# Performance work log

Measured on AMD Instinct MI355X. Metric: run time of the kernel, lower is better.

The kernel has to match this reference:

```python
import jax, jax.numpy as jnp
import numpy as np

B, T, C = 4, 2048, 1024
H, HS = 16, 64  # num_heads, head_size; H*HS == C

def setup_inputs() -> dict:
    key = jax.random.key(0)
    ks = jax.random.split(key, 6)
    s = 0.02
    x = jax.random.normal(ks[0], (B, T, C), dtype=jnp.float32)
    Wq = jax.random.normal(ks[1], (H, C, HS), dtype=jnp.float32) * s
    Wk = jax.random.normal(ks[2], (H, C, HS), dtype=jnp.float32) * s
    Wv = jax.random.normal(ks[3], (H, C, HS), dtype=jnp.float32) * s
    Wproj = jax.random.normal(ks[4], (C, C), dtype=jnp.float32) * s  # applied as out @ Wproj
    bproj = jax.random.normal(ks[5], (C,), dtype=jnp.float32) * s
    return {"x": x, "Wq": Wq, "Wk": Wk, "Wv": Wv, "Wproj": Wproj, "bproj": bproj}

def reference(x, Wq, Wk, Wv, Wproj, bproj):
    Bx, Tx, Cx = x.shape
    scale = Cx ** (-0.5)  # NOTE: original scales by n_embd, not head_size
    q = jnp.einsum('btc,hcd->bhtd', x, Wq)
    k = jnp.einsum('btc,hcd->bhtd', x, Wk)
    v = jnp.einsum('btc,hcd->bhtd', x, Wv)
    wei = jnp.einsum('bhtd,bhsd->bhts', q, k) * scale  # [B,H,T,T]
    causal = jnp.tril(jnp.ones((Tx, Tx), dtype=bool))
    wei = jnp.where(causal, wei, -jnp.inf)
    wei = jax.nn.softmax(wei, axis=-1)
    out = jnp.einsum('bhts,bhsd->bhtd', wei, v)
    out = out.transpose(0, 2, 1, 3).reshape(Bx, Tx, Cx)  # concat heads
    return out @ Wproj + bproj
```

## Files before the change

kernel.cpp:

```cpp
#include <hip/hip_runtime.h>


using u16    = unsigned short;
using bf16x8 = __attribute__((ext_vector_type(8))) short;
using bf16x4 = __attribute__((ext_vector_type(4))) short;
using f32x4  = __attribute__((ext_vector_type(4))) float;

#define MFMA_BF16(a, b, c) __builtin_amdgcn_mfma_f32_16x16x32_bf16((a), (b), (c), 0, 0, 0)

__device__ __forceinline__ f32x4 mfma16(bf16x4 a, bf16x4 b, f32x4 c) {
#if __has_builtin(__builtin_amdgcn_mfma_f32_16x16x16bf16_1k)
    return __builtin_amdgcn_mfma_f32_16x16x16bf16_1k(a, b, c, 0, 0, 0);
#elif __has_builtin(__builtin_amdgcn_mfma_f32_16x16x16_bf16)
    return __builtin_amdgcn_mfma_f32_16x16x16_bf16(a, b, c, 0, 0, 0);
#else
    asm("v_mfma_f32_16x16x16_bf16 %0, %1, %2, %0" : "+v"(c) : "v"(a), "v"(b));
    return c;
#endif
}

__device__ __forceinline__ u16 f2bf(float f) {
    union { float f; unsigned u; } v; v.f = f;
    unsigned u = v.u;
    u += 0x7FFFu + ((u >> 16) & 1u);
    return (u16)(u >> 16);
}
__device__ __forceinline__ short tbf(float f) {
    union { float f; unsigned u; } v; v.f = f;
    return (short)(v.u >> 16);
}

__device__ __forceinline__ void gl_lds16(const void* g, void* s) {
    __builtin_amdgcn_global_load_lds(
        (__attribute__((address_space(1))) void*)g,
        (__attribute__((address_space(3))) void*)s,
        16, 0, 0);
}

__global__ void cvt_x(const float* __restrict__ x, u16* __restrict__ xb, int n4) {
    int i = blockIdx.x * blockDim.x + threadIdx.x;
    if (i < n4) {
        float4 v = ((const float4*)x)[i];
        ushort4 o;
        o.x = f2bf(v.x); o.y = f2bf(v.y); o.z = f2bf(v.z); o.w = f2bf(v.w);
        ((ushort4*)xb)[i] = o;
    }
}

__global__ void transpose_w(const float* __restrict__ Wq, const float* __restrict__ Wk,
                            const float* __restrict__ Wv, u16* __restrict__ WT) {
    __shared__ float tile[64][65];
    const int tid = threadIdx.x;
    const int c0  = blockIdx.x * 64;
    const int h   = blockIdx.y;
    const int z   = blockIdx.z;
    const float* W = (z == 0 ? Wq : (z == 1 ? Wk : Wv)) + (size_t)h * 1024 * 64;
    u16* out = WT + (size_t)z * 1024 * 1024 + (size_t)h * 64 * 1024;
    #pragma unroll
    for (int i = 0; i < 16; ++i) {
        int idx = i * 256 + tid;
        int r = idx >> 6, d = idx & 63;
        tile[d][r] = W[(size_t)(c0 + r) * 64 + d];
    }
    __syncthreads();
    #pragma unroll
    for (int i = 0; i < 16; ++i) {
        int idx = i * 256 + tid;
        int d = idx >> 6, j = idx & 63;
        out[(size_t)d * 1024 + c0 + j] = f2bf(tile[d][j]);
    }
}

__global__ void transpose_p(const float* __restrict__ Wp, u16* __restrict__ WpT) {
    __shared__ float tile[64][65];
    const int tid = threadIdx.x;
    const int c0  = blockIdx.x * 64;
    const int n0  = blockIdx.y * 64;
    #pragma unroll
    for (int i = 0; i < 16; ++i) {
        int idx = i * 256 + tid;
        int r = idx >> 6, j = idx & 63;
        tile[j][r] = Wp[(size_t)(c0 + r) * 1024 + n0 + j];
    }
    __syncthreads();
    #pragma unroll
    for (int i = 0; i < 16; ++i) {
        int idx = i * 256 + tid;
        int r = idx >> 6, j = idx & 63;
        WpT[(size_t)(n0 + r) * 1024 + c0 + j] = f2bf(tile[r][j]);
    }
}

template <int MODE>
__global__ __launch_bounds__(256, 2)
void gemm_bt(const u16* __restrict__ A, const u16* __restrict__ Bt,
             u16* __restrict__ Oq, u16* __restrict__ Ok, u16* __restrict__ Ov,
             float* __restrict__ Op, const float* __restrict__ bias) {
    constexpr int K = 1024;
    __shared__ u16 As[128 * 32];
    __shared__ u16 Bs[128 * 32];
    const int tid  = threadIdx.x;
    const int w    = tid >> 6;
    const int lane = tid & 63;
    const int quad = lane >> 4;
    const int l16  = lane & 15;
    const int m0   = blockIdx.x * 128;
    const int n0   = blockIdx.y * 128;
    const u16* Bp  = (MODE == 0) ? (Bt + (size_t)blockIdx.z * 1024 * 1024) : Bt;

    const f32x4 zero = {0.f, 0.f, 0.f, 0.f};
    f32x4 acc[4][4];
    #pragma unroll
    for (int i = 0; i < 4; ++i)
        #pragma unroll
        for (int j = 0; j < 4; ++j) acc[i][j] = zero;

    const int wr = (w >> 1) * 64;
    const int wc = (w & 1) * 64;

    for (int k0 = 0; k0 < K; k0 += 32) {
        __syncthreads();
        #pragma unroll
        for (int i = 0; i < 2; ++i) {
            int c = i * 256 + tid;
            int row = c >> 2, ko = (c & 3) * 8;
            gl_lds16(A + (size_t)(m0 + row) * K + (k0 + ko), &As[(i * 256 + w * 64) * 8]);
        }
        #pragma unroll
        for (int i = 0; i < 2; ++i) {
            int c = i * 256 + tid;
            int row = c >> 2, ko = (c & 3) * 8;
            gl_lds16(Bp + (size_t)(n0 + row) * K + (k0 + ko), &Bs[(i * 256 + w * 64) * 8]);
        }
        __syncthreads();
        bf16x8 af[4], bfr[4];
        #pragma unroll
        for (int i = 0; i < 4; ++i)
            af[i] = *(const bf16x8*)&As[(wr + i * 16 + l16) * 32 + quad * 8];
        #pragma unroll
        for (int j = 0; j < 4; ++j)
            bfr[j] = *(const bf16x8*)&Bs[(wc + j * 16 + l16) * 32 + quad * 8];
        #pragma unroll
        for (int i = 0; i < 4; ++i)
            #pragma unroll
            for (int j = 0; j < 4; ++j)
                acc[i][j] = MFMA_BF16(af[i], bfr[j], acc[i][j]);
    }

    #pragma unroll
    for (int i = 0; i < 4; ++i) {
        #pragma unroll
        for (int j = 0; j < 4; ++j) {
            #pragma unroll
            for (int r = 0; r < 4; ++r) {
                const int m = m0 + wr + i * 16 + quad * 4 + r;
                const int n = n0 + wc + j * 16 + l16;
                const float v = acc[i][j][r];
                if (MODE == 0) {
                    const int b = m >> 11, t = m & 2047;
                    const int h = n >> 6, d = n & 63;
                    const int bh = b * 16 + h;
                    if (blockIdx.z == 0)
                        Oq[((size_t)bh * 2048 + t) * 64 + d] = f2bf(v * 0.03125f);
                    else if (blockIdx.z == 1)
                        Ok[((size_t)bh * 2048 + t) * 64 + d] = f2bf(v);
                    else
                        Ov[((size_t)bh * 64 + d) * 2048 + t] = f2bf(v);
                } else {
                    Op[(size_t)m * 1024 + n] = v + bias[n];
                }
            }
        }
    }
}

__global__ __launch_bounds__(256, 2)
void attn7(const u16* __restrict__ Q, const u16* __restrict__ Kg,
           const u16* __restrict__ Vt, u16* __restrict__ O) {
    __shared__ __align__(16) u16 Ks[2][2 * 128 * 32];
    __shared__ __align__(16) u16 VF[16 * 128 * 4];
    const int tid  = threadIdx.x;
    const int w    = tid >> 6;
    const int lane = tid & 63;
    const int quad = lane >> 4;
    const int l16  = lane & 15;
    const int bh   = blockIdx.y;
    const u16* Qp = Q  + (size_t)bh * 2048 * 64;
    const u16* Kp = Kg + (size_t)bh * 2048 * 64;
    const u16* Vp = Vt + (size_t)bh * 64 * 2048;
    const int b = bh >> 4, h = bh & 15;
    const float NEG_INF = -__builtin_inff();
    const f32x4 zero = {0.f, 0.f, 0.f, 0.f};
    const int vd = w * 16 + l16;

    #pragma unroll
    for (int ph = 0; ph < 2; ++ph) {
        const int tt = ph ? (int)blockIdx.x : 15 - (int)blockIdx.x;
        const int t0 = tt * 128;
        const int ns = tt + 1;

        bf16x8 bq[2][2];
        #pragma unroll
        for (int tf = 0; tf < 2; ++tf)
            #pragma unroll
            for (int kk = 0; kk < 2; ++kk)
                bq[tf][kk] = *(const bf16x8*)(Qp + (size_t)(t0 + w * 32 + tf * 16 + l16) * 64
                                              + kk * 32 + quad * 8);

        f32x4 oacc[4][2];
        float lsum[2] = {0.f, 0.f};
        #pragma unroll
        for (int df = 0; df < 4; ++df)
            #pragma unroll
            for (int tf = 0; tf < 2; ++tf) oacc[df][tf] = zero;

        __syncthreads();
        uint4 vr[4];
        #pragma unroll
        for (int i = 0; i < 4; ++i) {
            int c = i * 256 + tid;
            int kk = c >> 9, row = (c >> 2) & 127, q4 = c & 3;
            gl_lds16(Kp + (size_t)row * 64 + kk * 32 + q4 * 8,
                     &Ks[0][(size_t)(i * 256 + w * 64) * 8]);
        }
        #pragma unroll
        for (int r = 0; r < 4; ++r)
            vr[r] = *(const uint4*)(Vp + (size_t)vd * 2048 + (r * 4 + quad) * 8);

        for (int it = 0; it < ns; ++it) {
            const int s0 = it * 128;
            const u16* Kc = Ks[it & 1];
            __syncthreads();
            #pragma unroll
            for (int r = 0; r < 4; ++r) {
                const int uA = ((w * 4 + r) * 128) + (quad & 1) * 64 + l16 * 2
                               + ((quad >> 1) & 1);
                *(uint2*)&VF[(size_t)uA * 4]        = make_uint2(vr[r].x, vr[r].y);
                *(uint2*)&VF[(size_t)(uA + 32) * 4] = make_uint2(vr[r].z, vr[r].w);
            }
            __syncthreads();

            if (it + 1 < ns) {
                const int sn = s0 + 128;
                u16* Kn = Ks[(it + 1) & 1];
                #pragma unroll
                for (int i = 0; i < 4; ++i) {
                    int c = i * 256 + tid;
                    int kk = c >> 9, row = (c >> 2) & 127, q4 = c & 3;
                    gl_lds16(Kp + (size_t)(sn + row) * 64 + kk * 32 + q4 * 8,
                             &Kn[(size_t)(i * 256 + w * 64) * 8]);
                }
                #pragma unroll
                for (int r = 0; r < 4; ++r)
                    vr[r] = *(const uint4*)(Vp + (size_t)vd * 2048 + sn + (r * 4 + quad) * 8);
            }

            const bool diag = (it == ns - 1);
            bf16x4 bp[8][2];
            #pragma unroll
            for (int st = 0; st < 8; ++st) {
                bf16x8 ak0 = *(const bf16x8*)&Kc[(st * 16 + l16) * 32 + quad * 8];
                bf16x8 ak1 = *(const bf16x8*)&Kc[(128 * 32) + (st * 16 + l16) * 32 + quad * 8];
                #pragma unroll
                for (int tf = 0; tf < 2; ++tf) {
                    f32x4 s = MFMA_BF16(ak0, bq[tf][0], zero);
                    s = MFMA_BF16(ak1, bq[tf][1], s);
                    if (diag) {
                        #pragma unroll
                        for (int r = 0; r < 4; ++r) {
                            int ss = s0 + st * 16 + quad * 4 + r;
                            int t  = t0 + w * 32 + tf * 16 + l16;
                            if (ss > t) s[r] = NEG_INF;
                        }
                    }
                    float p0 = __expf(s[0]), p1 = __expf(s[1]);
                    float p2 = __expf(s[2]), p3 = __expf(s[3]);
                    lsum[tf] += (p0 + p1) + (p2 + p3);
                    bf16x4 bb; bb[0] = tbf(p0); bb[1] = tbf(p1);
                    bb[2] = tbf(p2); bb[3] = tbf(p3);
                    bp[st][tf] = bb;
                }
            }
            #pragma unroll
            for (int kcp = 0; kcp < 4; ++kcp)
                #pragma unroll
                for (int df = 0; df < 4; ++df) {
                    bf16x8 av = *(const bf16x8*)&VF[(size_t)(((df * 4 + kcp) * 128)
                                                    + quad * 32 + l16 * 2) * 4];
                    bf16x4 alo = __builtin_shufflevector(av, av, 0, 1, 2, 3);
                    bf16x4 ahi = __builtin_shufflevector(av, av, 4, 5, 6, 7);
                    #pragma unroll
                    for (int tf = 0; tf < 2; ++tf) {
                        oacc[df][tf] = mfma16(alo, bp[2 * kcp][tf], oacc[df][tf]);
                        oacc[df][tf] = mfma16(ahi, bp[2 * kcp + 1][tf], oacc[df][tf]);
                    }
                }
        }

        #pragma unroll
        for (int tf = 0; tf < 2; ++tf) {
            float s = lsum[tf];
            s += __shfl_xor(s, 16, 64);
            s += __shfl_xor(s, 32, 64);
            lsum[tf] = 1.0f / s;
        }
        #pragma unroll
        for (int df = 0; df < 4; ++df)
            #pragma unroll
            for (int tf = 0; tf < 2; ++tf)
                #pragma unroll
                for (int r = 0; r < 4; ++r) {
                    int t = t0 + w * 32 + tf * 16 + l16;
                    int d = df * 16 + quad * 4 + r;
                    O[((size_t)(b * 2048 + t)) * 1024 + h * 64 + d]
                        = f2bf(oacc[df][tf][r] * lsum[tf]);
                }
    }
}

extern "C" void kernel_launch(void* const* d_in, const int* in_sizes, int n_in,
                              void* d_out, int out_size, void* d_ws, size_t ws_size,
                              hipStream_t stream) {
    const float* x  = (const float*)d_in[0];
    const float* Wq = (const float*)d_in[1];
    const float* Wk = (const float*)d_in[2];
    const float* Wv = (const float*)d_in[3];
    const float* Wp = (const float*)d_in[4];
    const float* bp = (const float*)d_in[5];
    float* out = (float*)d_out;

    char* ws = (char*)d_ws;
    u16* Xb  = (u16*)(ws);
    u16* Xo  = (u16*)(ws);
    u16* WT  = (u16*)(ws + (16ull << 20));
    u16* WpT = (u16*)(ws + (22ull << 20));
    u16* Qw  = (u16*)(ws + (24ull << 20));
    u16* Kw  = (u16*)(ws + (40ull << 20));
    u16* Vw  = (u16*)(ws + (56ull << 20));

    cvt_x<<<8192, 256, 0, stream>>>(x, Xb, 8192 * 1024 / 4);
    transpose_w<<<dim3(16, 16, 3), 256, 0, stream>>>(Wq, Wk, Wv, WT);
    transpose_p<<<dim3(16, 16), 256, 0, stream>>>(Wp, WpT);
    gemm_bt<0><<<dim3(64, 8, 3), 256, 0, stream>>>(Xb, WT, Qw, Kw, Vw, nullptr, nullptr);
    attn7<<<dim3(8, 64), 256, 0, stream>>>(Qw, Kw, Vw, Xo);
    gemm_bt<1><<<dim3(64, 8, 1), 256, 0, stream>>>(Xo, WpT, nullptr, nullptr, nullptr, out, bp);
}
```

Baseline: 265.6 us.

## Rewrite projection GEMMs as 8-wave double-buffered pipelined kernel with LDS swizzle

Replaces the 256-thread 128x128 GEMM with a 512-thread 256x128 tile kernel that double-buffers K=64 LDS stages, overlaps async global-to-LDS loads with MFMA work through interleaved barriers and vmcnt waits, and XOR-swizzles LDS rows to reduce bank conflicts. It also raises wave priority around MFMA blocks. The goal is to hide global load latency and cut the per-iteration full syncs of the old loop, at the cost of more LDS per block and intricate barrier ordering that could be fragile.

```diff
diff --git a/kernel.cpp b/kernel.cpp
--- a/kernel.cpp
+++ b/kernel.cpp
@@ -91,22 +91,40 @@
     }
 }
 
+
+__device__ __forceinline__ void stage128(const u16* __restrict__ G, int grow0, int k0,
+                                         u16* lbase, int R0, int pstride,
+                                         int w, int lane) {
+    const int lrow = lane >> 2;
+    const int lcol = ((lane & 3) * 8) ^ ((lane >> 5) << 4);
+    #pragma unroll
+    for (int i = 0; i < 2; ++i) {
+        const int j  = 2 * w + i;
+        const int ks = j >> 3, rb = (j & 7) * 16;
+        const u16* sp = G + (size_t)(grow0 + rb + lrow) * 1024 + k0 + ks * 32 + lcol;
+        u16* dp = lbase + ks * pstride + (R0 + rb) * 32;
+        gl_lds16(sp, dp);
+    }
+}
+
 template <int MODE>
-__global__ __launch_bounds__(256, 2)
-void gemm_bt(const u16* __restrict__ A, const u16* __restrict__ Bt,
-             u16* __restrict__ Oq, u16* __restrict__ Ok, u16* __restrict__ Ov,
-             float* __restrict__ Op, const float* __restrict__ bias) {
-    constexpr int K = 1024;
-    __shared__ u16 As[128 * 32];
-    __shared__ u16 Bs[128 * 32];
+__global__ __launch_bounds__(512, 2)
+void gemm8(const u16* __restrict__ A, const u16* __restrict__ Bt,
+           u16* __restrict__ Oq, u16* __restrict__ Ok, u16* __restrict__ Ov,
+           float* __restrict__ Op, const float* __restrict__ bias) {
+    __shared__ __align__(16) u16 As[2][2 * 256 * 32];
+    __shared__ __align__(16) u16 Bs[2][2 * 128 * 32];
     const int tid  = threadIdx.x;
     const int w    = tid >> 6;
     const int lane = tid & 63;
     const int quad = lane >> 4;
     const int l16  = lane & 15;
-    const int m0   = blockIdx.x * 128;
+    const int wm   = w >> 1;
+    const int wn   = w & 1;
+    const int m0   = blockIdx.x * 256;
     const int n0   = blockIdx.y * 128;
     const u16* Bp  = (MODE == 0) ? (Bt + (size_t)blockIdx.z * 1024 * 1024) : Bt;
+    constexpr int NT = 16;
 
     const f32x4 zero = {0.f, 0.f, 0.f, 0.f};
     f32x4 acc[4][4];
@@ -115,36 +133,80 @@
         #pragma unroll
         for (int j = 0; j < 4; ++j) acc[i][j] = zero;
 
-    const int wr = (w >> 1) * 64;
-    const int wc = (w & 1) * 64;
-
-    for (int k0 = 0; k0 < K; k0 += 32) {
-        __syncthreads();
-        #pragma unroll
-        for (int i = 0; i < 2; ++i) {
-            int c = i * 256 + tid;
-            int row = c >> 2, ko = (c & 3) * 8;
-            gl_lds16(A + (size_t)(m0 + row) * K + (k0 + ko), &As[(i * 256 + w * 64) * 8]);
-        }
-        #pragma unroll
-        for (int i = 0; i < 2; ++i) {
-            int c = i * 256 + tid;
-            int row = c >> 2, ko = (c & 3) * 8;
-            gl_lds16(Bp + (size_t)(n0 + row) * K + (k0 + ko), &Bs[(i * 256 + w * 64) * 8]);
-        }
-        __syncthreads();
-        bf16x8 af[4], bfr[4];
-        #pragma unroll
-        for (int i = 0; i < 4; ++i)
-            af[i] = *(const bf16x8*)&As[(wr + i * 16 + l16) * 32 + quad * 8];
-        #pragma unroll
-        for (int j = 0; j < 4; ++j)
-            bfr[j] = *(const bf16x8*)&Bs[(wc + j * 16 + l16) * 32 + quad * 8];
-        #pragma unroll
-        for (int i = 0; i < 4; ++i)
-            #pragma unroll
-            for (int j = 0; j < 4; ++j)
-                acc[i][j] = MFMA_BF16(af[i], bfr[j], acc[i][j]);
+    auto rdA = [&](const u16* Ab, bf16x8 (&d)[2][2], int mfb) {
+        #pragma unroll
+        for (int mf = 0; mf < 2; ++mf) {
+            const int row  = wm * 64 + (mfb + mf) * 16 + l16;
+            const int base = row * 32 + quad * 8;
+            const int sw   = ((row >> 3) & 1) << 4;
+            #pragma unroll
+            for (int ks = 0; ks < 2; ++ks)
+                d[mf][ks] = *(const bf16x8*)&Ab[(ks * 8192 + base) ^ sw];
+        }
+    };
+    auto rdB = [&](const u16* Bb, bf16x8 (&d)[2][2], int nfb) {
+        #pragma unroll
+        for (int nf = 0; nf < 2; ++nf) {
+            const int row  = wn * 64 + (nfb + nf) * 16 + l16;
+            const int base = row * 32 + quad * 8;
+            const int sw   = ((row >> 3) & 1) << 4;
+            #pragma unroll
+            for (int ks = 0; ks < 2; ++ks)
+                d[nf][ks] = *(const bf16x8*)&Bb[(ks * 4096 + base) ^ sw];
+        }
+    };
+    auto mm = [&](bf16x8 (&av)[2][2], bf16x8 (&bv)[2][2], int mb, int nb) {
+        __builtin_amdgcn_s_setprio(1);
+        #pragma unroll
+        for (int ks = 0; ks < 2; ++ks)
+            #pragma unroll
+            for (int mf = 0; mf < 2; ++mf)
+                #pragma unroll
+                for (int nf = 0; nf < 2; ++nf)
+                    acc[mb + mf][nb + nf] =
+                        MFMA_BF16(av[mf][ks], bv[nf][ks], acc[mb + mf][nb + nf]);
+        __builtin_amdgcn_s_setprio(0);
+    };
+
+    stage128(A,  m0,       0,  As[0], 0,   8192, w, lane);
+    stage128(A,  m0 + 128, 0,  As[0], 128, 8192, w, lane);
+    stage128(Bp, n0,       0,  Bs[0], 0,   4096, w, lane);
+    stage128(A,  m0,       64, As[1], 0,   8192, w, lane);
+    stage128(Bp, n0,       64, Bs[1], 0,   4096, w, lane);
+    asm volatile("s_waitcnt vmcnt(4)");
+    __builtin_amdgcn_s_barrier();
+
+    for (int t = 0; t < NT; ++t) {
+        const u16* Ab = As[t & 1];
+        const u16* Bb = Bs[t & 1];
+        bf16x8 a[2][2], blo[2][2], bhi[2][2];
+
+        rdA(Ab, a, 0);
+        rdB(Bb, blo, 0);
+        if (t + 1 < NT)
+            stage128(A, m0 + 128, (t + 1) * 64, As[(t + 1) & 1], 128, 8192, w, lane);
+        __builtin_amdgcn_s_barrier();
+        mm(a, blo, 0, 0);
+        __builtin_amdgcn_s_barrier();
+
+        rdB(Bb, bhi, 2);
+        __builtin_amdgcn_s_barrier();
+        mm(a, bhi, 0, 2);
+        __builtin_amdgcn_s_barrier();
+
+        rdA(Ab, a, 2);
+        if (t + 2 < NT)
+            stage128(Bp, n0, (t + 2) * 64, Bs[t & 1], 0, 4096, w, lane);
+        __builtin_amdgcn_s_barrier();
+        mm(a, bhi, 2, 2);
+        __builtin_amdgcn_s_barrier();
+
+        if (t + 2 < NT)
+            stage128(A, m0, (t + 2) * 64, As[t & 1], 0, 8192, w, lane);
+        __builtin_amdgcn_s_barrier();
+        mm(a, blo, 2, 0);
+        asm volatile("s_waitcnt vmcnt(4)");
+        __builtin_amdgcn_s_barrier();
     }
 
     #pragma unroll
@@ -153,8 +215,8 @@
         for (int j = 0; j < 4; ++j) {
             #pragma unroll
             for (int r = 0; r < 4; ++r) {
-                const int m = m0 + wr + i * 16 + quad * 4 + r;
-                const int n = n0 + wc + j * 16 + l16;
+                const int m = m0 + wm * 64 + i * 16 + quad * 4 + r;
+                const int n = n0 + wn * 64 + j * 16 + l16;
                 const float v = acc[i][j][r];
                 if (MODE == 0) {
                     const int b = m >> 11, t = m & 2047;
@@ -341,7 +403,7 @@
     cvt_x<<<8192, 256, 0, stream>>>(x, Xb, 8192 * 1024 / 4);
     transpose_w<<<dim3(16, 16, 3), 256, 0, stream>>>(Wq, Wk, Wv, WT);
     transpose_p<<<dim3(16, 16), 256, 0, stream>>>(Wp, WpT);
-    gemm_bt<0><<<dim3(64, 8, 3), 256, 0, stream>>>(Xb, WT, Qw, Kw, Vw, nullptr, nullptr);
+    gemm8<0><<<dim3(32, 8, 3), 512, 0, stream>>>(Xb, WT, Qw, Kw, Vw, nullptr, nullptr);
     attn7<<<dim3(8, 64), 256, 0, stream>>>(Qw, Kw, Vw, Xo);
-    gemm_bt<1><<<dim3(64, 8, 1), 256, 0, stream>>>(Xo, WpT, nullptr, nullptr, nullptr, out, bp);
-}
+    gemm8<1><<<dim3(32, 8), 512, 0, stream>>>(Xo, WpT, nullptr, nullptr, nullptr, out, bp);
+}
```

Measured after the change: 288.2 us. +8.5%, slower.
